# Optimization experiments

Measured on AMD Instinct MI355X. Metric: run time of the kernel, lower is better.

The kernel has to match this reference:

```python
import jax
import jax.numpy as jnp
import numpy as np

LATENT = 4096
LABEL = 512
CLUSTERING_N = 1

# Sign with straight-through gradient (matches torch Sign.backward = identity)
@jax.custom_vjp
def sign_ste(x):
    return (x >= 0).astype(x.dtype) * 2 - 1

def _sign_fwd(x):
    return sign_ste(x), None

def _sign_bwd(_, g):
    return (g,)

sign_ste.defvjp(_sign_fwd, _sign_bwd)

# MaxOneHot: keep only argmax entry; backward passes 0.5*grad at argmax
@jax.custom_vjp
def max_onehot(x):
    idx = jnp.argmax(x)
    return jnp.zeros_like(x).at[idx].set(x[idx])

def _moh_fwd(x):
    idx = jnp.argmax(x)
    return jnp.zeros_like(x).at[idx].set(x[idx]), idx

def _moh_bwd(idx, g):
    return (0.5 * jnp.zeros_like(g).at[idx].set(g[idx]),)

max_onehot.defvjp(_moh_fwd, _moh_bwd)


def setup_inputs() -> dict:
    key = jax.random.key(0)
    k1, k2 = jax.random.split(key)
    s = jax.random.normal(k1, (LATENT,), dtype=jnp.float32)
    # matches torch init: 2*rand - 1 in (-1, 1)
    llv = 2.0 * jax.random.uniform(k2, (LABEL, LATENT), dtype=jnp.float32) - 1.0
    return {"s": s, "label_latent_vectors": llv}


def _hopfield_forward(s, llv):
    # weight build: x = sign(clamp(llv)); W = sum_i outer(x_i - rho) / label_size, zero diag
    x = sign_ste(jnp.clip(llv, -1.0, 1.0))          # [LABEL, LATENT]
    rho = jnp.mean(x)
    temp = x - rho                                   # [LABEL, LATENT]
    weight = (temp.T @ temp) / jnp.asarray(x.shape[0], x.dtype)  # [LATENT, LATENT]
    weight = weight - jnp.diag(jnp.diag(weight))

    # Gauss-Seidel sweep: sequential update s[i] = sign(W[i] . stop_grad(s))
    def step(s_carry, wi_i):
        wi, i = wi_i
        v = jnp.dot(wi, jax.lax.stop_gradient(s_carry))
        return s_carry.at[i].set(sign_ste(v)), None

    idxs = jnp.arange(weight.shape[0])
    for _ in range(CLUSTERING_N):
        s, _ = jax.lax.scan(step, s, (weight, idxs))

    scores = jnp.abs(s @ x.T) / jnp.asarray(s.shape[0], s.dtype)  # [LABEL]
    return max_onehot(scores)


def reference(s, label_latent_vectors):
    return _hopfield_forward(s, label_latent_vectors)
```

## Files before the change

### kernel.cpp

```cpp
#include <hip/hip_runtime.h>
#include <hip/hip_bf16.h>


#define OFF_COLB   0u
#define OFF_XBITS  (256u<<10)
#define OFF_XBW    (512u<<10)
#define OFF_KF     (768u<<10)
#define OFF_BCORR  (1792u<<10)
#define OFF_U      (1808u<<10)
#define OFF_CST    (1936u<<10)
#define OFF_P0     (2000u<<10)
#define OFF_SBITS  (2002u<<10)
#define OFF_CNT    (2003u<<10)
#define OFF_HDR    (2019u<<10)
#define OFF_BS0    (2020u<<10)
#define OFF_BS0C   (2021u<<10)

template<int CTRL, int RMASK>
__device__ __forceinline__ float dpp_add(float x){
  int t = __builtin_amdgcn_update_dpp(0, __float_as_int(x), CTRL, RMASK, 0xf, true);
  return x + __int_as_float(t);
}
__device__ __forceinline__ float wave_allsum(float x){
  x = dpp_add<0x111,0xf>(x);
  x = dpp_add<0x112,0xf>(x);
  x = dpp_add<0x114,0xf>(x);
  x = dpp_add<0x118,0xf>(x);
  x = dpp_add<0x142,0xa>(x);
  x = dpp_add<0x143,0xc>(x);
  return __int_as_float(__builtin_amdgcn_readlane(__float_as_int(x), 63));
}

__global__ void k_xbits(const float* __restrict__ llv, unsigned long long* __restrict__ xbits,
                        unsigned long long* __restrict__ xbitsW){
  int w = threadIdx.x >> 6, lane = threadIdx.x & 63;
  int l = blockIdx.x*4 + w;
  unsigned long long myword = 0;
  for (int c = 0; c < 64; ++c){
    float v = llv[(size_t)l*4096 + c*64 + lane];
    unsigned long long b = __ballot(v >= 0.0f);
    if (c == lane) myword = b;
  }
  xbits[(size_t)l*64 + lane] = myword;
  xbitsW[(size_t)lane*512 + l] = myword;
}

__global__ void k_bitT(const unsigned long long* __restrict__ xbits,
                       unsigned long long* __restrict__ colbitsP){
  int li = blockIdx.x;
  int ii = blockIdx.y;
  int lane = threadIdx.x;
  unsigned long long w = xbits[(size_t)(li*64 + lane)*64 + ii];
  unsigned long long myw = 0;
  for (int j = 0; j < 64; ++j){
    unsigned long long b = __ballot((w >> j) & 1ull);
    if (j == lane) myw = b;
  }
  colbitsP[(size_t)li*4096 + ii*64 + lane] = myw;
}

__global__ void k_colc(const unsigned long long* __restrict__ colbitsP, int* __restrict__ colcnt){
  int i = blockIdx.x*256 + threadIdx.x;
  int c = 0;
  #pragma unroll
  for (int wl = 0; wl < 8; ++wl) c += __popcll(colbitsP[(size_t)wl*4096 + i]);
  colcnt[i] = c;
}

__global__ void k_rho(const int* __restrict__ colcnt, float* __restrict__ hdr){
  __shared__ int sh[256];
  int tid = threadIdx.x;
  int s = 0;
  for (int k = tid; k < 4096; k += 256) s += colcnt[k];
  sh[tid] = s; __syncthreads();
  for (int st = 128; st > 0; st >>= 1){
    if (tid < st) sh[tid] += sh[tid + st];
    __syncthreads();
  }
  if (tid == 0){
    int num = 2*sh[0] - 2097152;
    hdr[0] = (float)num * (1.0f/2097152.0f);
  }
}

__global__ void k_const(const int* __restrict__ colcnt, const float* __restrict__ hdr,
                        const float* __restrict__ s0, float4* __restrict__ cst){
  int i = blockIdx.x*256 + threadIdx.x;
  float rho = hdr[0];
  float c  = (float)(2*colcnt[i] - 512);
  float r2 = rho*rho;
  float q  = 512.0f + 512.0f*r2 - 2.0f*rho*c;
  float s  = s0[i];
  float4 o;
  o.x = q * s;
  o.y = rho*c - 512.0f*r2;
  o.z = 1.0f - s;
  o.w = c;
  cst[i] = o;
}

__global__ void k_kdiag(const unsigned long long* __restrict__ colbitsP,
                        const float4* __restrict__ cst, const float* __restrict__ s0,
                        const float* __restrict__ hdr,
                        float* __restrict__ Kf, float* __restrict__ baseCorr,
                        float* __restrict__ blkS0, float* __restrict__ blkS0C){
  __shared__ unsigned long long cb[8][64];
  __shared__ float Kl[64][64];
  __shared__ float cs[64], ss[64];
  int b = blockIdx.x, i0 = b*64, tid = threadIdx.x;
  for (int k = tid; k < 512; k += 256)
    cb[k>>6][k&63] = colbitsP[(size_t)(k>>6)*4096 + i0 + (k&63)];
  if (tid < 64){ cs[tid] = cst[i0+tid].w; ss[tid] = s0[i0+tid]; }
  __syncthreads();
  float rho = hdr[0];
  float r2t = 512.0f*rho*rho;
  #pragma unroll
  for (int k = 0; k < 16; ++k){
    int q = tid*16 + k;
    int t = q >> 6, j = q & 63;
    int acc = 0;
    #pragma unroll
    for (int wl = 0; wl < 8; ++wl) acc += __popcll(cb[wl][t] ^ cb[wl][j]);
    float G = (float)(512 - 2*acc);
    float kf = G - rho*(cs[t]+cs[j]) + r2t;
    Kl[t][j] = kf;
    Kf[(size_t)b*4096 + q] = kf;
  }
  __syncthreads();
  if (tid < 64){
    float bc = 0.0f;
    for (int j = 0; j < tid; ++j) bc = fmaf(ss[j], Kl[tid][j], bc);
    baseCorr[i0 + tid] = bc;
  }
  if (tid == 64){
    float a = 0.0f, b2 = 0.0f;
    for (int j = 0; j < 64; ++j){ a += ss[j]; b2 = fmaf(ss[j], cs[j], b2); }
    blkS0[b] = a; blkS0C[b] = b2;
  }
}

__global__ void k_u(const unsigned long long* __restrict__ xbits, const float* __restrict__ s0,
                    float* __restrict__ U){
  __shared__ float s0l[64];
  int b = blockIdx.x, l = threadIdx.x;
  if (l < 64) s0l[l] = s0[b*64 + l];
  __syncthreads();
  unsigned long long w = xbits[(size_t)l*64 + b];
  unsigned int lo = (unsigned)w, hi = (unsigned)(w >> 32);
  unsigned int nlo = ~lo, nhi = ~hi;
  float acc = 0.0f;
  #pragma unroll
  for (int j = 0; j < 32; ++j){
    unsigned int m = (nlo << (31-j)) & 0x80000000u;
    acc += __uint_as_float(__float_as_uint(s0l[j]) ^ m);
  }
  #pragma unroll
  for (int j = 0; j < 32; ++j){
    unsigned int m = (nhi << (31-j)) & 0x80000000u;
    acc += __uint_as_float(__float_as_uint(s0l[32+j]) ^ m);
  }
  U[(size_t)b*512 + l] = acc;
}

__global__ void k_pinit(const float* __restrict__ llv, const float* __restrict__ s0,
                        float* __restrict__ p0){
  int l = blockIdx.x, lane = threadIdx.x;
  float acc = 0.0f;
  for (int c = 0; c < 64; ++c){
    float v = llv[(size_t)l*4096 + c*64 + lane];
    float sg = (v >= 0.0f) ? 1.0f : -1.0f;
    acc = fmaf(sg, s0[c*64 + lane], acc);
  }
  float tot = wave_allsum(acc);
  if (lane == 0) p0[l] = tot;
}

#define STP(KVAL, J) { \
  int vi_ = __builtin_amdgcn_readlane(__float_as_int(v), (J)); \
  float sg2_ = (vi_ < 0) ? -1.0f : 1.0f; \
  sg_ |= ((unsigned long long)((~((unsigned)vi_)) >> 31)) << (J); \
  v = fmaf(sg2_, (KVAL), v); }
#define STP4(Q, J0) STP(Q.x,(J0)+0) STP(Q.y,(J0)+1) STP(Q.z,(J0)+2) STP(Q.w,(J0)+3)
#define LDK4(P, F0) { P##0 = Kp[((F0)+0)^sw]; P##1 = Kp[((F0)+1)^sw]; \
                      P##2 = Kp[((F0)+2)^sw]; P##3 = Kp[((F0)+3)^sw]; }
#define PROC16(P, J0) STP4(P##0,(J0)) STP4(P##1,(J0)+4) STP4(P##2,(J0)+8) STP4(P##3,(J0)+12)

#define ACC1(F, W, JS) { \
  unsigned int m_ = ((~(W)) << (31-(JS))) & 0x80000000u; \
  acc += __uint_as_float(__float_as_uint(F) ^ m_); }

__global__ __launch_bounds__(512, 1)
void k_sweep3(const unsigned long long* __restrict__ colbitsP,
              const unsigned long long* __restrict__ xbitsW,
              const float* __restrict__ Kf, const float* __restrict__ baseCorr,
              const float* __restrict__ blkS0, const float* __restrict__ blkS0C,
              const float* __restrict__ U, const float4* __restrict__ cst,
              const float* __restrict__ p0, const float* __restrict__ s0,
              const float* __restrict__ hdr, unsigned long long* __restrict__ sbits)
{
  __shared__ float Kl[2][64][64];
  __shared__ unsigned long long cbl[2][8][64];
  __shared__ unsigned long long xbl[2][512];
  __shared__ float Ul[2][512];
  __shared__ float4 cstl[2][64];
  __shared__ float bcl[2][64];
  __shared__ float bs0l[64], bscl[64];
  __shared__ float p[512];
  __shared__ float part[8][64];
  __shared__ float red[512];
  __shared__ unsigned long long sig;

  int tid = threadIdx.x, g = tid >> 6, t = tid & 63;
  float rho = hdr[0];

  p[tid] = p0[tid];
  red[tid] = p0[tid];
  if (tid < 64){ bs0l[tid] = blkS0[tid]; bscl[tid] = blkS0C[tid]; }
  __syncthreads();
  for (int st = 256; st > 0; st >>= 1){ if (tid < st) red[tid] += red[tid+st]; __syncthreads(); }
  float Preg = red[0];
  __syncthreads();
  { float a = 0.0f; for (int k = 0; k < 8; ++k) a += s0[tid*8 + k]; red[tid] = a; }
  __syncthreads();
  for (int st = 256; st > 0; st >>= 1){ if (tid < st) red[tid] += red[tid+st]; __syncthreads(); }
  float Treg = red[0];
  __syncthreads();

  for (int grp = 0; grp < 32; ++grp){
    {
      const float4* Ks = (const float4*)(Kf + (size_t)grp*8192);
      #pragma unroll
      for (int k = 0; k < 4; ++k){
        int e = tid + k*512;
        float4 vv = Ks[e];
        int gie = e >> 10, row = (e >> 4) & 63, f = e & 15;
        *((float4*)&Kl[gie][row][0] + (f ^ (row & 15))) = vv;
      }
      #pragma unroll
      for (int k = 0; k < 2; ++k){
        int e = tid + k*512;
        int run = e >> 6, tt = e & 63, gie = run >> 3, wl = run & 7;
        cbl[gie][wl][tt] = colbitsP[(size_t)wl*4096 + (grp*2+gie)*64 + tt];
      }
      const unsigned long long* xs = xbitsW + (size_t)grp*1024;
      #pragma unroll
      for (int k = 0; k < 2; ++k){
        int e = tid + k*512;
        ((unsigned long long*)xbl)[e] = xs[e];
      }
      const float* Us = U + (size_t)grp*1024;
      #pragma unroll
      for (int k = 0; k < 2; ++k){
        int e = tid + k*512;
        ((float*)Ul)[e] = Us[e];
      }
      if (tid < 128){
        ((float4*)cstl)[tid] = cst[grp*128 + tid];
        ((float*)bcl)[tid]   = baseCorr[grp*128 + tid];
      }
    }
    __syncthreads();

    #pragma unroll
    for (int gi = 0; gi < 2; ++gi){
      int b = grp*2 + gi;
      {
        unsigned long long w = cbl[gi][g][t];
        unsigned int lo = (unsigned)w, hi = (unsigned)(w >> 32);
        const float4* pw = (const float4*)(p + g*64);
        float acc = 0.0f;
        #pragma unroll
        for (int f = 0; f < 16; ++f){
          float4 q = pw[f];
          if (f < 8){
            ACC1(q.x, lo, 4*f+0) ACC1(q.y, lo, 4*f+1)
            ACC1(q.z, lo, 4*f+2) ACC1(q.w, lo, 4*f+3)
          } else {
            ACC1(q.x, hi, 4*f-32) ACC1(q.y, hi, 4*f-31)
            ACC1(q.z, hi, 4*f-30) ACC1(q.w, hi, 4*f-29)
          }
        }
        part[g][t] = acc;
      }
      __syncthreads();

      if (g == 0){
        const float4* Kp = (const float4*)&Kl[gi][t][0];
        int sw = t & 15;
        float4 KA0,KA1,KA2,KA3, KB0,KB1,KB2,KB3;
        LDK4(KA, 0); LDK4(KB, 4);
        float S = 0.0f;
        #pragma unroll
        for (int gg = 0; gg < 8; ++gg) S += part[gg][t];
        float4 cc = cstl[gi][t];
        float bc_ = bcl[gi][t];
        float v = S - cc.x - rho*Preg - cc.y*Treg - bc_;
        unsigned long long sg_ = 0ull;
        PROC16(KA, 0);  LDK4(KA, 8);
        PROC16(KB, 16); LDK4(KB, 12);
        PROC16(KA, 32);
        PROC16(KB, 48);
        if (t == 0){ sig = sg_; sbits[b] = sg_; }
        float sv = ((sg_ >> t) & 1ull) ? cc.w : -cc.w;
        float sc = wave_allsum(sv);
        int pcs = __popcll(sg_);
        Preg += sc - bscl[b];
        Treg += (float)(2*pcs - 64) - bs0l[b];
      }
      __syncthreads();
      {
        unsigned long long sgv = sig;
        int pc = __popcll(xbl[gi][tid] ^ sgv);
        p[tid] = p[tid] + (float)(64 - 2*pc) - Ul[gi][tid];
      }
      __syncthreads();
    }
  }
}

__global__ void k_scores(const unsigned long long* __restrict__ xbits,
                         const unsigned long long* __restrict__ sbits,
                         float* __restrict__ out){
  __shared__ unsigned long long sb[64];
  __shared__ int bestkey;
  int tid = threadIdx.x;
  if (tid < 64) sb[tid] = sbits[tid];
  if (tid == 0) bestkey = -1;
  __syncthreads();
  int acc = 0;
  #pragma unroll
  for (int w = 0; w < 64; ++w)
    acc += __popcll(xbits[(size_t)tid*64 + w] ^ sb[w]);
  int dot = 4096 - 2*acc;
  int ad  = dot < 0 ? -dot : dot;
  int key = (ad << 10) | (511 - tid);
  atomicMax(&bestkey, key);
  __syncthreads();
  int bl = 511 - (bestkey & 1023);
  float val = (float)(bestkey >> 10) * (1.0f/4096.0f);
  out[tid] = (tid == bl) ? val : 0.0f;
}

extern "C" void kernel_launch(void* const* d_in, const int* in_sizes, int n_in,
                              void* d_out, int out_size, void* d_ws, size_t ws_size,
                              hipStream_t stream){
  const float* s0  = (const float*)d_in[0];
  const float* llv = (const float*)d_in[1];
  float* out = (float*)d_out;
  char* ws = (char*)d_ws;

  unsigned long long* colbitsP = (unsigned long long*)(ws + OFF_COLB);
  unsigned long long* xbits    = (unsigned long long*)(ws + OFF_XBITS);
  unsigned long long* xbitsW   = (unsigned long long*)(ws + OFF_XBW);
  float*  Kf    = (float*)(ws + OFF_KF);
  float*  bcorr = (float*)(ws + OFF_BCORR);
  float*  U     = (float*)(ws + OFF_U);
  float4* cst   = (float4*)(ws + OFF_CST);
  float*  p0    = (float*)(ws + OFF_P0);
  unsigned long long* sbits = (unsigned long long*)(ws + OFF_SBITS);
  int*    colcnt = (int*)(ws + OFF_CNT);
  float*  hdr   = (float*)(ws + OFF_HDR);
  float*  bS0   = (float*)(ws + OFF_BS0);
  float*  bS0C  = (float*)(ws + OFF_BS0C);

  k_xbits<<<128, 256, 0, stream>>>(llv, xbits, xbitsW);
  k_bitT<<<dim3(8, 64), 64, 0, stream>>>(xbits, colbitsP);
  k_colc<<<16, 256, 0, stream>>>(colbitsP, colcnt);
  k_rho<<<1, 256, 0, stream>>>(colcnt, hdr);
  k_const<<<16, 256, 0, stream>>>(colcnt, hdr, s0, cst);
  k_kdiag<<<64, 256, 0, stream>>>(colbitsP, cst, s0, hdr, Kf, bcorr, bS0, bS0C);
  k_u<<<64, 512, 0, stream>>>(xbits, s0, U);
  k_pinit<<<512, 64, 0, stream>>>(llv, s0, p0);
  k_sweep3<<<1, 512, 0, stream>>>(colbitsP, xbitsW, Kf, bcorr, bS0, bS0C, U, cst, p0, s0, hdr, sbits);
  k_scores<<<1, 512, 0, stream>>>(xbits, sbits, out);
}
```

Measured before the change: 220.1 us.

## Overlap next-block partial sums with current block's serial sweep via cross-block Gram correction

```diff
diff --git a/kernel.cpp b/kernel.cpp
--- a/kernel.cpp
+++ b/kernel.cpp
@@ -15,6 +15,8 @@
 #define OFF_HDR    (2019u<<10)
 #define OFF_BS0    (2020u<<10)
 #define OFF_BS0C   (2021u<<10)
+#define OFF_GCX    (2048u<<10)
+#define OFF_VC     (2560u<<10)
 
 template<int CTRL, int RMASK>
 __device__ __forceinline__ float dpp_add(float x){
@@ -47,9 +49,7 @@
 
 __global__ void k_bitT(const unsigned long long* __restrict__ xbits,
                        unsigned long long* __restrict__ colbitsP){
-  int li = blockIdx.x;
-  int ii = blockIdx.y;
-  int lane = threadIdx.x;
+  int li = blockIdx.x, ii = blockIdx.y, lane = threadIdx.x;
   unsigned long long w = xbits[(size_t)(li*64 + lane)*64 + ii];
   unsigned long long myw = 0;
   for (int j = 0; j < 64; ++j){
@@ -99,17 +99,22 @@
   cst[i] = o;
 }
 
-__global__ void k_kdiag(const unsigned long long* __restrict__ colbitsP,
-                        const float4* __restrict__ cst, const float* __restrict__ s0,
-                        const float* __restrict__ hdr,
-                        float* __restrict__ Kf, float* __restrict__ baseCorr,
-                        float* __restrict__ blkS0, float* __restrict__ blkS0C){
-  __shared__ unsigned long long cb[8][64];
+__global__ void k_kdiag2(const unsigned long long* __restrict__ colbitsP,
+                         const float4* __restrict__ cst, const float* __restrict__ s0,
+                         const float* __restrict__ hdr,
+                         float* __restrict__ Kf, float* __restrict__ baseCorr,
+                         float* __restrict__ blkS0, float* __restrict__ blkS0C,
+                         short* __restrict__ Gcx, float* __restrict__ Vc){
+  __shared__ unsigned long long cb[8][64], cb2[8][64];
   __shared__ float Kl[64][64];
+  __shared__ float Gl[64][64];
   __shared__ float cs[64], ss[64];
   int b = blockIdx.x, i0 = b*64, tid = threadIdx.x;
-  for (int k = tid; k < 512; k += 256)
-    cb[k>>6][k&63] = colbitsP[(size_t)(k>>6)*4096 + i0 + (k&63)];
+  int bn = (b + 1 < 64) ? (b + 1) : 63;
+  for (int k = tid; k < 512; k += 256){
+    cb [k>>6][k&63] = colbitsP[(size_t)(k>>6)*4096 + i0     + (k&63)];
+    cb2[k>>6][k&63] = colbitsP[(size_t)(k>>6)*4096 + bn*64  + (k&63)];
+  }
   if (tid < 64){ cs[tid] = cst[i0+tid].w; ss[tid] = s0[i0+tid]; }
   __syncthreads();
   float rho = hdr[0];
@@ -118,19 +123,27 @@
   for (int k = 0; k < 16; ++k){
     int q = tid*16 + k;
     int t = q >> 6, j = q & 63;
-    int acc = 0;
+    int acc = 0, acc2 = 0;
     #pragma unroll
-    for (int wl = 0; wl < 8; ++wl) acc += __popcll(cb[wl][t] ^ cb[wl][j]);
+    for (int wl = 0; wl < 8; ++wl){
+      acc  += __popcll(cb [wl][t] ^ cb[wl][j]);
+      acc2 += __popcll(cb2[wl][t] ^ cb[wl][j]);
+    }
     float G = (float)(512 - 2*acc);
     float kf = G - rho*(cs[t]+cs[j]) + r2t;
     Kl[t][j] = kf;
     Kf[(size_t)b*4096 + q] = kf;
+    int G2 = (b == 63) ? 0 : (512 - 2*acc2);
+    Gl[t][j] = (float)G2;
+    Gcx[(size_t)b*4096 + q] = (short)G2;
   }
   __syncthreads();
   if (tid < 64){
-    float bc = 0.0f;
+    float bc = 0.0f, vc = 0.0f;
     for (int j = 0; j < tid; ++j) bc = fmaf(ss[j], Kl[tid][j], bc);
+    for (int j = 0; j < 64; ++j)  vc = fmaf(ss[j], Gl[tid][j], vc);
     baseCorr[i0 + tid] = bc;
+    Vc[i0 + tid] = vc;
   }
   if (tid == 64){
     float a = 0.0f, b2 = 0.0f;
@@ -189,24 +202,44 @@
   unsigned int m_ = ((~(W)) << (31-(JS))) & 0x80000000u; \
   acc += __uint_as_float(__float_as_uint(F) ^ m_); }
 
+#define SPREB(C, COLBASE, DEST) { \
+  unsigned long long w_ = colbitsP[(size_t)(C)*4096 + (size_t)(COLBASE) + t]; \
+  unsigned int lo = (unsigned)w_, hi = (unsigned)(w_ >> 32); \
+  const float4* pw_ = (const float4*)(p + (C)*64); \
+  float acc = 0.0f; \
+  _Pragma("unroll") \
+  for (int f = 0; f < 16; ++f){ \
+    float4 q = pw_[f]; \
+    if (f < 8){ ACC1(q.x, lo, 4*f+0) ACC1(q.y, lo, 4*f+1) \
+                ACC1(q.z, lo, 4*f+2) ACC1(q.w, lo, 4*f+3) } \
+    else      { ACC1(q.x, hi, 4*f-32) ACC1(q.y, hi, 4*f-31) \
+                ACC1(q.z, hi, 4*f-30) ACC1(q.w, hi, 4*f-29) } \
+  } \
+  DEST = acc; }
+
+#define ADDG1(WORD, SH, KIDX) { \
+  float f_ = (float)(short)((WORD) >> (SH)); \
+  unsigned int m_ = (((sgv >> (j0 + (KIDX))) & 1ull) ? 0u : 0x80000000u); \
+  dacc += __uint_as_float(__float_as_uint(f_) ^ m_); }
+
 __global__ __launch_bounds__(512, 1)
-void k_sweep3(const unsigned long long* __restrict__ colbitsP,
+void k_sweep4(const unsigned long long* __restrict__ colbitsP,
               const unsigned long long* __restrict__ xbitsW,
               const float* __restrict__ Kf, const float* __restrict__ baseCorr,
               const float* __restrict__ blkS0, const float* __restrict__ blkS0C,
               const float* __restrict__ U, const float4* __restrict__ cst,
               const float* __restrict__ p0, const float* __restrict__ s0,
-              const float* __restrict__ hdr, unsigned long long* __restrict__ sbits)
+              const float* __restrict__ hdr, const short* __restrict__ Gcx,
+              const float* __restrict__ Vc, unsigned long long* __restrict__ sbits)
 {
   __shared__ float Kl[2][64][64];
-  __shared__ unsigned long long cbl[2][8][64];
-  __shared__ unsigned long long xbl[2][512];
-  __shared__ float Ul[2][512];
+  __shared__ short Gcl[2][64][64];
   __shared__ float4 cstl[2][64];
   __shared__ float bcl[2][64];
+  __shared__ float Vcl[2][64];
   __shared__ float bs0l[64], bscl[64];
   __shared__ float p[512];
-  __shared__ float part[8][64];
+  __shared__ float part[2][8][64];
   __shared__ float red[512];
   __shared__ unsigned long long sig;
 
@@ -224,6 +257,8 @@
   __syncthreads();
   for (int st = 256; st > 0; st >>= 1){ if (tid < st) red[tid] += red[tid+st]; __syncthreads(); }
   float Treg = red[0];
+  __syncthreads();
+  SPREB(g, 0, part[0][g][t]);
   __syncthreads();
 
   for (int grp = 0; grp < 32; ++grp){
@@ -236,27 +271,17 @@
         int gie = e >> 10, row = (e >> 4) & 63, f = e & 15;
         *((float4*)&Kl[gie][row][0] + (f ^ (row & 15))) = vv;
       }
+      const unsigned long long* Gs = (const unsigned long long*)(Gcx + (size_t)grp*8192);
       #pragma unroll
-      for (int k = 0; k < 2; ++k){
+      for (int k = 0; k < 4; ++k){
         int e = tid + k*512;
-        int run = e >> 6, tt = e & 63, gie = run >> 3, wl = run & 7;
-        cbl[gie][wl][tt] = colbitsP[(size_t)wl*4096 + (grp*2+gie)*64 + tt];
-      }
-      const unsigned long long* xs = xbitsW + (size_t)grp*1024;
-      #pragma unroll
-      for (int k = 0; k < 2; ++k){
-        int e = tid + k*512;
-        ((unsigned long long*)xbl)[e] = xs[e];
-      }
-      const float* Us = U + (size_t)grp*1024;
-      #pragma unroll
-      for (int k = 0; k < 2; ++k){
-        int e = tid + k*512;
-        ((float*)Ul)[e] = Us[e];
+        int gie = e >> 10, rem = e & 1023, tt = rem >> 4, wi = rem & 15;
+        ((unsigned long long*)&Gcl[gie][tt][0])[ ((wi>>1) ^ (tt&7))*2 + (wi&1) ] = Gs[e];
       }
       if (tid < 128){
         ((float4*)cstl)[tid] = cst[grp*128 + tid];
         ((float*)bcl)[tid]   = baseCorr[grp*128 + tid];
+        ((float*)Vcl)[tid]   = Vc[grp*128 + tid];
       }
     }
     __syncthreads();
@@ -264,25 +289,9 @@
     #pragma unroll
     for (int gi = 0; gi < 2; ++gi){
       int b = grp*2 + gi;
-      {
-        unsigned long long w = cbl[gi][g][t];
-        unsigned int lo = (unsigned)w, hi = (unsigned)(w >> 32);
-        const float4* pw = (const float4*)(p + g*64);
-        float acc = 0.0f;
-        #pragma unroll
-        for (int f = 0; f < 16; ++f){
-          float4 q = pw[f];
-          if (f < 8){
-            ACC1(q.x, lo, 4*f+0) ACC1(q.y, lo, 4*f+1)
-            ACC1(q.z, lo, 4*f+2) ACC1(q.w, lo, 4*f+3)
-          } else {
-            ACC1(q.x, hi, 4*f-32) ACC1(q.y, hi, 4*f-31)
-            ACC1(q.z, hi, 4*f-30) ACC1(q.w, hi, 4*f-29)
-          }
-        }
-        part[g][t] = acc;
-      }
-      __syncthreads();
+      int pb = b & 1, nb = pb ^ 1;
+      unsigned long long xw_ = xbitsW[(size_t)b*512 + tid];
+      float uu_ = U[(size_t)b*512 + tid];
 
       if (g == 0){
         const float4* Kp = (const float4*)&Kl[gi][t][0];
@@ -291,7 +300,7 @@
         LDK4(KA, 0); LDK4(KB, 4);
         float S = 0.0f;
         #pragma unroll
-        for (int gg = 0; gg < 8; ++gg) S += part[gg][t];
+        for (int gg = 0; gg < 8; ++gg) S += part[pb][gg][t];
         float4 cc = cstl[gi][t];
         float bc_ = bcl[gi][t];
         float v = S - cc.x - rho*Preg - cc.y*Treg - bc_;
@@ -306,12 +315,30 @@
         int pcs = __popcll(sg_);
         Preg += sc - bscl[b];
         Treg += (float)(2*pcs - 64) - bs0l[b];
+      } else if (b < 63){
+        int c1 = g - 1;
+        SPREB(c1, (b+1)*64, part[nb][c1][t]);
+        if (g == 1){
+          SPREB(7, (b+1)*64, part[nb][7][t]);
+        }
       }
       __syncthreads();
+
       {
         unsigned long long sgv = sig;
-        int pc = __popcll(xbl[gi][tid] ^ sgv);
-        p[tid] = p[tid] + (float)(64 - 2*pc) - Ul[gi][tid];
+        int pc = __popcll(xw_ ^ sgv);
+        p[tid] = p[tid] + (float)(64 - 2*pc) - uu_;
+        if (b < 63){
+          const int4* Gr = (const int4*)&Gcl[gi][t][0];
+          int4 raw = Gr[g ^ (t & 7)];
+          int j0 = g*8;
+          float dacc = (g == 0) ? -Vcl[gi][t] : 0.0f;
+          ADDG1(raw.x, 0, 0) ADDG1(raw.x, 16, 1)
+          ADDG1(raw.y, 0, 2) ADDG1(raw.y, 16, 3)
+          ADDG1(raw.z, 0, 4) ADDG1(raw.z, 16, 5)
+          ADDG1(raw.w, 0, 6) ADDG1(raw.w, 16, 7)
+          part[nb][g][t] += dacc;
+        }
       }
       __syncthreads();
     }
@@ -362,15 +389,17 @@
   float*  hdr   = (float*)(ws + OFF_HDR);
   float*  bS0   = (float*)(ws + OFF_BS0);
   float*  bS0C  = (float*)(ws + OFF_BS0C);
+  short*  Gcx   = (short*)(ws + OFF_GCX);
+  float*  Vc    = (float*)(ws + OFF_VC);
 
   k_xbits<<<128, 256, 0, stream>>>(llv, xbits, xbitsW);
   k_bitT<<<dim3(8, 64), 64, 0, stream>>>(xbits, colbitsP);
   k_colc<<<16, 256, 0, stream>>>(colbitsP, colcnt);
   k_rho<<<1, 256, 0, stream>>>(colcnt, hdr);
   k_const<<<16, 256, 0, stream>>>(colcnt, hdr, s0, cst);
-  k_kdiag<<<64, 256, 0, stream>>>(colbitsP, cst, s0, hdr, Kf, bcorr, bS0, bS0C);
+  k_kdiag2<<<64, 256, 0, stream>>>(colbitsP, cst, s0, hdr, Kf, bcorr, bS0, bS0C, Gcx, Vc);
   k_u<<<64, 512, 0, stream>>>(xbits, s0, U);
   k_pinit<<<512, 64, 0, stream>>>(llv, s0, p0);
-  k_sweep3<<<1, 512, 0, stream>>>(colbitsP, xbitsW, Kf, bcorr, bS0, bS0C, U, cst, p0, s0, hdr, sbits);
+  k_sweep4<<<1, 512, 0, stream>>>(colbitsP, xbitsW, Kf, bcorr, bS0, bS0C, U, cst, p0, s0, hdr, Gcx, Vc, sbits);
   k_scores<<<1, 512, 0, stream>>>(xbits, sbits, out);
 }
```

Result: no change. 223.5 us (+1.5%).
